# Optimization experiments

Hardware: AMD Instinct MI355X
Metric: run time of the kernel (lower is better)

The kernel has to match this reference:

```python
import jax, jax.numpy as jnp
import numpy as np

N_NODES = 50000
N_EDGES = 800000
D_IN = 512
D_OUT = 256


def setup_inputs() -> dict:
    key = jax.random.key(0)
    k1, k2, k3 = jax.random.split(key, 3)
    x = jax.random.normal(k1, (N_NODES, D_IN), dtype=jnp.float32)
    edge_index = jax.random.randint(k2, (2, N_EDGES), 0, N_NODES, dtype=jnp.int64)
    # Glorot-style init for the GCN weight, zero bias (PyG defaults)
    W = jax.random.normal(k3, (D_IN, D_OUT), dtype=jnp.float32) * (1.0 / np.sqrt(D_IN))
    b = jnp.zeros((D_OUT,), dtype=jnp.float32)
    return {"x": x, "edge_index": edge_index, "W": W, "b": b}


def reference(x, edge_index, W, b):
    N = x.shape[0]
    # 1) dense linear transform (the compute-heavy GEMM)
    xw = x @ W  # [N, d_out]

    # 2) add self-loops (PyG GCNConv default)
    loop = jnp.arange(N, dtype=edge_index.dtype)
    row = jnp.concatenate([edge_index[0], loop])  # sources
    col = jnp.concatenate([edge_index[1], loop])  # targets

    # 3) symmetric normalization deg^{-1/2} on targets (in-degree incl. self-loops)
    deg = jax.ops.segment_sum(jnp.ones_like(col, dtype=xw.dtype), col, num_segments=N)
    dinv = jnp.where(deg > 0, jax.lax.rsqrt(deg), 0.0)
    norm = dinv[row] * dinv[col]  # [E+N]

    # 4) gather source features, scale, scatter-add to targets
    msgs = xw[row] * norm[:, None]  # [E+N, d_out]
    agg = jax.ops.segment_sum(msgs, col, num_segments=N)  # [N, d_out]

    # 5) bias + ReLU (dropout is identity in eval mode)
    return jax.nn.relu(agg + b)
```

## Files before the change

kernel.cpp:

```cpp
#include <hip/hip_runtime.h>
#include <hip/hip_bf16.h>

#define N_NODES 50000
#define N_EDGES 800000
#define D_IN    512
#define D_OUT   256
#define NBLK_SCAN ((N_NODES + 1023) / 1024)
#define GEMM_NWG (((N_NODES + 127) / 128) * 2)
#define GEMM_Q   (GEMM_NWG / 8)
#define GEMM_R   (GEMM_NWG % 8)
#define GATH_CHUNKS ((N_NODES + 63) / 64)

typedef short s8v  __attribute__((ext_vector_type(8)));
typedef float f32x4 __attribute__((ext_vector_type(4)));

__device__ __forceinline__ unsigned short bf16b(float f) {
    __hip_bfloat16 h = __float2bfloat16(f);
    return *reinterpret_cast<unsigned short*>(&h);
}
__device__ __forceinline__ float bflo(unsigned u) { return __uint_as_float(u << 16); }
__device__ __forceinline__ float bfhi(unsigned u) { return __uint_as_float(u & 0xffff0000u); }

#define GLD16(gp, lp)                                                           \
    __builtin_amdgcn_global_load_lds(                                           \
        (const __attribute__((address_space(1))) unsigned int*)(const void*)(gp),\
        (__attribute__((address_space(3))) unsigned int*)(void*)(lp), 16, 0, 0)

__device__ __forceinline__ int wave_incl_scan(int v, int lane) {
    #pragma unroll
    for (int d = 1; d < 64; d <<= 1) {
        int u = __shfl_up(v, d, 64);
        if (lane >= d) v += u;
    }
    return v;
}

__global__ void k_wt(const float* __restrict__ W, unsigned short* __restrict__ Wt,
                     int* __restrict__ cnt4) {
    int k = blockIdx.x;
    int n = threadIdx.x;
    Wt[(size_t)n * D_IN + k] = bf16b(W[(size_t)k * D_OUT + n]);
    int t = (blockIdx.x * 256 + threadIdx.x) * 2;
    if (t < 4 * N_NODES) {
        cnt4[t] = 0;
        if (t + 1 < 4 * N_NODES) cnt4[t + 1] = 0;
    }
}


__global__ void k_count(const int* __restrict__ col, int* __restrict__ cnt4) {
    int i = (blockIdx.x * 256 + threadIdx.x) * 2;
    if (i < N_EDGES) {
        int2 c = *(const int2*)&col[i];
        atomicAdd(&cnt4[(i & 3) * N_NODES + c.x], 1);
        atomicAdd(&cnt4[((i + 1) & 3) * N_NODES + c.y], 1);
    }
}

__launch_bounds__(256)
__global__ void k_scan1(const int* __restrict__ cnt4, int* __restrict__ bsum) {
    const int t = threadIdx.x, b = blockIdx.x;
    const int idx = b * 1024 + t * 4;
    int s = 0;
    if (idx < N_NODES) {
        #pragma unroll
        for (int q = 0; q < 4; ++q) {
            int4 v = *(const int4*)&cnt4[q * N_NODES + idx];
            s += (v.x + v.y) + (v.z + v.w);
        }
    }
    #pragma unroll
    for (int d = 1; d < 64; d <<= 1) s += __shfl_xor(s, d, 64);
    __shared__ int ws[4];
    if ((t & 63) == 0) ws[t >> 6] = s;
    __syncthreads();
    if (t == 0) bsum[b] = ws[0] + ws[1] + ws[2] + ws[3];
}

__launch_bounds__(256)
__global__ void k_scan3(const int* __restrict__ cnt4, const int* __restrict__ bsum,
                        int* __restrict__ row_ptr, float* __restrict__ dinv,
                        int* __restrict__ cursor4) {
    const int t = threadIdx.x, b = blockIdx.x;
    const int lane = t & 63, wv = t >> 6;
    const int idx = b * 1024 + t * 4;
    int4 vq[4];
    int4 tot = make_int4(0, 0, 0, 0);
    if (idx < N_NODES) {
        #pragma unroll
        for (int q = 0; q < 4; ++q) {
            vq[q] = *(const int4*)&cnt4[q * N_NODES + idx];
            tot.x += vq[q].x; tot.y += vq[q].y;
            tot.z += vq[q].z; tot.w += vq[q].w;
        }
    } else {
        #pragma unroll
        for (int q = 0; q < 4; ++q) vq[q] = make_int4(0, 0, 0, 0);
    }
    int s = (tot.x + tot.y) + (tot.z + tot.w);
    int isc = wave_incl_scan(s, lane);
    __shared__ int wsum[4];
    __shared__ int s_boff;
    if (lane == 63) wsum[wv] = isc;
    if (t < 64) {
        int u = (t < b) ? bsum[t] : 0;
        #pragma unroll
        for (int d = 1; d < 64; d <<= 1) u += __shfl_xor(u, d, 64);
        if (t == 0) s_boff = u;
    }
    __syncthreads();
    int off = s_boff;
    #pragma unroll
    for (int i = 0; i < 4; ++i)
        if (i < wv) off += wsum[i];
    int p0 = off + isc - s;
    int p1 = p0 + tot.x;
    int p2 = p1 + tot.y;
    int p3 = p2 + tot.z;
    if (idx < N_NODES) {
        row_ptr[idx + 0] = p0; dinv[idx + 0] = rsqrtf(1.f + (float)tot.x);
        row_ptr[idx + 1] = p1; dinv[idx + 1] = rsqrtf(1.f + (float)tot.y);
        row_ptr[idx + 2] = p2; dinv[idx + 2] = rsqrtf(1.f + (float)tot.z);
        row_ptr[idx + 3] = p3; dinv[idx + 3] = rsqrtf(1.f + (float)tot.w);
        int4 run = make_int4(p0, p1, p2, p3);
        #pragma unroll
        for (int q = 0; q < 4; ++q) {
            *(int4*)&cursor4[q * N_NODES + idx] = run;
            run.x += vq[q].x; run.y += vq[q].y;
            run.z += vq[q].z; run.w += vq[q].w;
        }
    }
    if (b == 0 && t == 0) row_ptr[N_NODES] = N_EDGES;
}

__global__ void k_fill(const int* __restrict__ row, const int* __restrict__ col,
                       int* __restrict__ cursor4, int* __restrict__ csr_src) {
    int i = (blockIdx.x * 256 + threadIdx.x) * 2;
    if (i < N_EDGES) {
        int2 c = *(const int2*)&col[i];
        int2 r = *(const int2*)&row[i];
        int p0 = atomicAdd(&cursor4[(i & 3) * N_NODES + c.x], 1);
        csr_src[p0] = r.x;
        int p1 = atomicAdd(&cursor4[((i + 1) & 3) * N_NODES + c.y], 1);
        csr_src[p1] = r.y;
    }
}

__launch_bounds__(256)
__global__ void k_gemm(const float* __restrict__ A,
                       const unsigned short* __restrict__ Wt,
                       const float* __restrict__ dinv,
                       unsigned short* __restrict__ yb)
{
    __shared__ __align__(16) float          As[128 * 64];
    __shared__ __align__(16) unsigned short Bs[128 * 64];

    int orig = blockIdx.x;
    int xcd = orig % 8, pos = orig / 8;
    int wg = (xcd < GEMM_R) ? xcd * (GEMM_Q + 1) + pos
                            : GEMM_R * (GEMM_Q + 1) + (xcd - GEMM_R) * GEMM_Q + pos;
    const int nt = wg & 1;
    const int mt = wg >> 1;
    const int m0 = mt * 128;
    const int n0 = nt * 128;

    const int t  = threadIdx.x;
    const int w  = t >> 6;
    const int l  = t & 63;
    const int wm = (w >> 1) * 64;
    const int wn = (w & 1) * 64;
    const int lr = l & 15;
    const int lk = l >> 4;

    size_t aoff[8];
    #pragma unroll
    for (int i = 0; i < 8; ++i) {
        int row = m0 + w * 32 + i * 4 + (l >> 4);
        if (row >= N_NODES) row = 0;
        int sslot = (l & 15) ^ (row & 7);
        aoff[i] = (size_t)row * D_IN + sslot * 4;
    }
    const int srow = l >> 3;
    const int srcj = (l & 7) ^ srow;
    size_t boff[4];
    #pragma unroll
    for (int i = 0; i < 4; ++i) {
        int g = w * 4 + i;
        int bn = n0 + g * 8 + srow;
        boff[i] = (size_t)bn * D_IN + srcj * 8;
    }

    f32x4 acc[4][4] = {};

    for (int kk = 0; kk < D_IN; kk += 64) {
        #pragma unroll
        for (int i = 0; i < 8; ++i)
            GLD16(&A[aoff[i] + kk], (char*)As + (w * 32 + i * 4) * 256);
        #pragma unroll
        for (int i = 0; i < 4; ++i)
            GLD16(&Wt[boff[i] + kk], (char*)Bs + (w * 4 + i) * 1024);
        __syncthreads();

        #pragma unroll
        for (int ks = 0; ks < 2; ++ks) {
            s8v af[4], bfr[4];
            #pragma unroll
            for (int f = 0; f < 4; ++f) {
                int row = wm + f * 16 + lr;
                int a   = (ks * 4 + lk) * 2;
                int s0  = a ^ (lr & 7);
                int s1  = (a + 1) ^ (lr & 7);
                const char* pr = (const char*)As + row * 256;
                float4 x0 = *(const float4*)(pr + s0 * 16);
                float4 x1 = *(const float4*)(pr + s1 * 16);
                union { s8v v; unsigned short h[8]; } u;
                u.h[0] = bf16b(x0.x); u.h[1] = bf16b(x0.y);
                u.h[2] = bf16b(x0.z); u.h[3] = bf16b(x0.w);
                u.h[4] = bf16b(x1.x); u.h[5] = bf16b(x1.y);
                u.h[6] = bf16b(x1.z); u.h[7] = bf16b(x1.w);
                af[f] = u.v;
            }
            const int kb = (ks * 64 + lk * 16) ^ ((lr & 7) << 4);
            #pragma unroll
            for (int f = 0; f < 4; ++f)
                bfr[f] = *(const s8v*)((const char*)Bs + ((wn + f * 16 + lr) * 128 + kb));
            #pragma unroll
            for (int fm = 0; fm < 4; ++fm)
                #pragma unroll
                for (int fn = 0; fn < 4; ++fn)
                    acc[fm][fn] = __builtin_amdgcn_mfma_f32_16x16x32_bf16(
                        af[fm], bfr[fn], acc[fm][fn], 0, 0, 0);
        }
        __syncthreads();
    }

    #pragma unroll
    for (int fm = 0; fm < 4; ++fm) {
        #pragma unroll
        for (int j = 0; j < 4; ++j) {
            int row = m0 + wm + fm * 16 + lk * 4 + j;
            if (row < N_NODES) {
                float s = dinv[row];
                #pragma unroll
                for (int fn = 0; fn < 4; ++fn) {
                    int col = n0 + wn + fn * 16 + lr;
                    size_t off = (size_t)(col >> 5) * (N_NODES * 32)
                               + (size_t)row * 32 + (col & 31);
                    yb[off] = bf16b(acc[fm][fn][j] * s);
                }
            }
        }
    }
}

__device__ __forceinline__ void add8(float* acc, uint4 q) {
    unsigned x;
    x = q.x; acc[0] += bflo(x); acc[1] += bfhi(x);
    x = q.y; acc[2] += bflo(x); acc[3] += bfhi(x);
    x = q.z; acc[4] += bflo(x); acc[5] += bfhi(x);
    x = q.w; acc[6] += bflo(x); acc[7] += bfhi(x);
}

__launch_bounds__(256)
__global__ void k_gather(const int* __restrict__ row_ptr, const int* __restrict__ csr_src,
                         const unsigned short* __restrict__ yb,
                         const float* __restrict__ dinv,
                         const float* __restrict__ bias, float* __restrict__ out)
{
    const int s     = blockIdx.x & 7;
    const int chunk = blockIdx.x >> 3;
    const int g     = threadIdx.x >> 2;
    const int cs    = threadIdx.x & 3;
    const int c     = chunk * 64 + g;
    if (c >= N_NODES) return;

    const uint4* t4 = (const uint4*)(yb + (size_t)s * N_NODES * 32);

    float acc[8] = {0.f,0.f,0.f,0.f,0.f,0.f,0.f,0.f};

    const int e0 = row_ptr[c];
    const int e1 = row_ptr[c + 1];
    for (int i = e0; i < e1; i += 4) {
        int idx[4];
        #pragma unroll
        for (int j = 0; j < 4; ++j) {
            int p = i + j;
            idx[j] = csr_src[p < e1 ? p : e1 - 1];
        }
        uint4 v[4];
        #pragma unroll
        for (int j = 0; j < 4; ++j) v[j] = t4[(size_t)idx[j] * 4 + cs];
        #pragma unroll
        for (int j = 0; j < 4; ++j)
            if (i + j < e1) add8(acc, v[j]);
    }

    add8(acc, t4[(size_t)c * 4 + cs]);

    const float sc = dinv[c];
    const int colb = s * 32 + cs * 8;
    float4 b0 = *(const float4*)&bias[colb];
    float4 b1 = *(const float4*)&bias[colb + 4];
    float4 o0, o1;
    o0.x = fmaxf(fmaf(acc[0], sc, b0.x), 0.f);
    o0.y = fmaxf(fmaf(acc[1], sc, b0.y), 0.f);
    o0.z = fmaxf(fmaf(acc[2], sc, b0.z), 0.f);
    o0.w = fmaxf(fmaf(acc[3], sc, b0.w), 0.f);
    o1.x = fmaxf(fmaf(acc[4], sc, b1.x), 0.f);
    o1.y = fmaxf(fmaf(acc[5], sc, b1.y), 0.f);
    o1.z = fmaxf(fmaf(acc[6], sc, b1.z), 0.f);
    o1.w = fmaxf(fmaf(acc[7], sc, b1.w), 0.f);
    float* dst = &out[(size_t)c * D_OUT + colb];
    *(float4*)dst       = o0;
    *(float4*)(dst + 4) = o1;
}

extern "C" void kernel_launch(void* const* d_in, const int* in_sizes, int n_in,
                              void* d_out, int out_size, void* d_ws, size_t ws_size,
                              hipStream_t stream) {
    const float* x   = (const float*)d_in[0];
    const int*   ei  = (const int*)d_in[1];
    const float* W   = (const float*)d_in[2];
    const float* b   = (const float*)d_in[3];
    float*       out = (float*)d_out;

    const int* row = ei;
    const int* col = ei + N_EDGES;

    char* p = (char*)d_ws;
    unsigned short* yb = (unsigned short*)p;  p += (size_t)N_NODES * D_OUT * 2;
    unsigned short* Wt = (unsigned short*)p;  p += (size_t)D_OUT * D_IN * 2;
    int*   csr_src = (int*)p;                 p += (size_t)N_EDGES * 4;
    int*   cnt4    = (int*)p;                 p += (size_t)4 * N_NODES * 4;
    int*   row_ptr = (int*)p;                 p += (size_t)(N_NODES + 4) * 4;
    int*   cursor4 = (int*)p;                 p += (size_t)4 * N_NODES * 4;
    float* dinv    = (float*)p;               p += (size_t)N_NODES * 4;
    int*   bsum    = (int*)p;                 p += (size_t)NBLK_SCAN * 4;

    k_wt   <<<D_IN, D_OUT, 0, stream>>>(W, Wt, cnt4);
    k_count<<<(N_EDGES / 2 + 255) / 256, 256, 0, stream>>>(col, cnt4);
    k_scan1<<<NBLK_SCAN, 256, 0, stream>>>(cnt4, bsum);
    k_scan3<<<NBLK_SCAN, 256, 0, stream>>>(cnt4, bsum, row_ptr, dinv, cursor4);
    k_fill <<<(N_EDGES / 2 + 255) / 256, 256, 0, stream>>>(row, col, cursor4, csr_src);

    k_gemm<<<GEMM_NWG, 256, 0, stream>>>(x, Wt, dinv, yb);

    k_gather<<<GATH_CHUNKS * 8, 256, 0, stream>>>(row_ptr, csr_src, yb, dinv, b, out);
}
```

Before: 192.6 us.

## Assign one wavefront per destination node in gather with shuffle reduction

The gather kernel now maps a full 64-lane wavefront to each destination node and feature slice, with 16 edge slots of 4 lanes each, instead of 4 lanes per node. Each slot walks every 16th edge, with the next index prefetched one iteration ahead, and the partial sums are combined by xor shuffles. This is meant to expose more memory-level parallelism and spread the irregular degree load across lanes rather than serialising each node's edges. In exchange it launches 16x more threads, adds 32 shuffle adds per lane, and leaves most lanes idle on low-degree nodes. It also drops the bounds check and relies on N_NODES being divisible by 4.

```diff
diff --git a/kernel.cpp b/kernel.cpp
--- a/kernel.cpp
+++ b/kernel.cpp
@@ -9,7 +9,6 @@
 #define GEMM_NWG (((N_NODES + 127) / 128) * 2)
 #define GEMM_Q   (GEMM_NWG / 8)
 #define GEMM_R   (GEMM_NWG % 8)
-#define GATH_CHUNKS ((N_NODES + 63) / 64)
 
 typedef short s8v  __attribute__((ext_vector_type(8)));
 typedef float f32x4 __attribute__((ext_vector_type(4)));
@@ -267,52 +266,62 @@
                          const float* __restrict__ dinv,
                          const float* __restrict__ bias, float* __restrict__ out)
 {
-    const int s     = blockIdx.x & 7;
-    const int chunk = blockIdx.x >> 3;
-    const int g     = threadIdx.x >> 2;
-    const int cs    = threadIdx.x & 3;
-    const int c     = chunk * 64 + g;
-    if (c >= N_NODES) return;
+    const int s    = blockIdx.x & 7;
+    const int c    = (blockIdx.x >> 3) * 4 + (threadIdx.x >> 6);
+    const int l    = threadIdx.x & 63;
+    const int slot = l >> 2;
+    const int cs   = l & 3;
 
     const uint4* t4 = (const uint4*)(yb + (size_t)s * N_NODES * 32);
-
-    float acc[8] = {0.f,0.f,0.f,0.f,0.f,0.f,0.f,0.f};
 
     const int e0 = row_ptr[c];
     const int e1 = row_ptr[c + 1];
-    for (int i = e0; i < e1; i += 4) {
-        int idx[4];
-        #pragma unroll
-        for (int j = 0; j < 4; ++j) {
-            int p = i + j;
-            idx[j] = csr_src[p < e1 ? p : e1 - 1];
-        }
-        uint4 v[4];
-        #pragma unroll
-        for (int j = 0; j < 4; ++j) v[j] = t4[(size_t)idx[j] * 4 + cs];
-        #pragma unroll
-        for (int j = 0; j < 4; ++j)
-            if (i + j < e1) add8(acc, v[j]);
-    }
-
-    add8(acc, t4[(size_t)c * 4 + cs]);
-
-    const float sc = dinv[c];
-    const int colb = s * 32 + cs * 8;
-    float4 b0 = *(const float4*)&bias[colb];
-    float4 b1 = *(const float4*)&bias[colb + 4];
-    float4 o0, o1;
-    o0.x = fmaxf(fmaf(acc[0], sc, b0.x), 0.f);
-    o0.y = fmaxf(fmaf(acc[1], sc, b0.y), 0.f);
-    o0.z = fmaxf(fmaf(acc[2], sc, b0.z), 0.f);
-    o0.w = fmaxf(fmaf(acc[3], sc, b0.w), 0.f);
-    o1.x = fmaxf(fmaf(acc[4], sc, b1.x), 0.f);
-    o1.y = fmaxf(fmaf(acc[5], sc, b1.y), 0.f);
-    o1.z = fmaxf(fmaf(acc[6], sc, b1.z), 0.f);
-    o1.w = fmaxf(fmaf(acc[7], sc, b1.w), 0.f);
-    float* dst = &out[(size_t)c * D_OUT + colb];
-    *(float4*)dst       = o0;
-    *(float4*)(dst + 4) = o1;
+
+    uint4 sv = t4[(size_t)c * 4 + cs];
+
+    float acc[8] = {0.f,0.f,0.f,0.f,0.f,0.f,0.f,0.f};
+
+    int i = e0;
+    int idx = 0;
+    if (e1 > e0) {
+        int p = e0 + slot;
+        idx = csr_src[p < e1 ? p : e1 - 1];
+    }
+    while (i < e1) {
+        uint4 v = t4[(size_t)idx * 4 + cs];
+        int ni = i + 16;
+        int np = ni + slot;
+        int nidx = csr_src[np < e1 ? np : e1 - 1];
+        if (i + slot < e1) add8(acc, v);
+        i = ni;
+        idx = nidx;
+    }
+    if (slot == 0) add8(acc, sv);
+
+    #pragma unroll
+    for (int d = 4; d < 64; d <<= 1)
+        #pragma unroll
+        for (int u = 0; u < 8; ++u)
+            acc[u] += __shfl_xor(acc[u], d, 64);
+
+    if (slot == 0) {
+        const float sc = dinv[c];
+        const int colb = s * 32 + cs * 8;
+        float4 b0 = *(const float4*)&bias[colb];
+        float4 b1 = *(const float4*)&bias[colb + 4];
+        float4 o0, o1;
+        o0.x = fmaxf(fmaf(acc[0], sc, b0.x), 0.f);
+        o0.y = fmaxf(fmaf(acc[1], sc, b0.y), 0.f);
+        o0.z = fmaxf(fmaf(acc[2], sc, b0.z), 0.f);
+        o0.w = fmaxf(fmaf(acc[3], sc, b0.w), 0.f);
+        o1.x = fmaxf(fmaf(acc[4], sc, b1.x), 0.f);
+        o1.y = fmaxf(fmaf(acc[5], sc, b1.y), 0.f);
+        o1.z = fmaxf(fmaf(acc[6], sc, b1.z), 0.f);
+        o1.w = fmaxf(fmaf(acc[7], sc, b1.w), 0.f);
+        float* dst = &out[(size_t)c * D_OUT + colb];
+        *(float4*)dst       = o0;
+        *(float4*)(dst + 4) = o1;
+    }
 }
 
 extern "C" void kernel_launch(void* const* d_in, const int* in_sizes, int n_in,
@@ -345,5 +354,5 @@
 
     k_gemm<<<GEMM_NWG, 256, 0, stream>>>(x, Wt, dinv, yb);
 
-    k_gather<<<GATH_CHUNKS * 8, 256, 0, stream>>>(row_ptr, csr_src, yb, dinv, b, out);
-}
+    k_gather<<<(N_NODES / 4) * 8, 256, 0, stream>>>(row_ptr, csr_src, yb, dinv, b, out);
+}
```

Measured after the change: 267.9 us. 39.1% more time.

## Double-buffer GEMM K-tiles with async LDS loads and vmcnt waits

Applied to the files above, without the earlier changes.

Restructures the GEMM main loop from single-buffered 64-wide K tiles to double-buffered 32-wide K tiles. The next tile's global-to-LDS loads are issued while the current one is computed, and partial vmcnt waits with raw s_barrier replace full __syncthreads. The intent is to hide global load latency behind the MFMA work. In exchange it has twice as many barriers per K, new swizzle patterns, and relies on the hand-counted vmcnt being correct.

```diff
diff --git a/kernel.cpp b/kernel.cpp
--- a/kernel.cpp
+++ b/kernel.cpp
@@ -152,8 +152,8 @@
                        const float* __restrict__ dinv,
                        unsigned short* __restrict__ yb)
 {
-    __shared__ __align__(16) float          As[128 * 64];
-    __shared__ __align__(16) unsigned short Bs[128 * 64];
+    __shared__ __align__(16) float          As[2 * 128 * 32];
+    __shared__ __align__(16) unsigned short Bs[2 * 128 * 32];
 
     int orig = blockIdx.x;
     int xcd = orig % 8, pos = orig / 8;
@@ -172,67 +172,86 @@
     const int lr = l & 15;
     const int lk = l >> 4;
 
-    size_t aoff[8];
-    #pragma unroll
-    for (int i = 0; i < 8; ++i) {
-        int row = m0 + w * 32 + i * 4 + (l >> 4);
-        if (row >= N_NODES) row = 0;
-        int sslot = (l & 15) ^ (row & 7);
-        aoff[i] = (size_t)row * D_IN + sslot * 4;
-    }
-    const int srow = l >> 3;
-    const int srcj = (l & 7) ^ srow;
-    size_t boff[4];
+    size_t aoff[4];
     #pragma unroll
     for (int i = 0; i < 4; ++i) {
-        int g = w * 4 + i;
-        int bn = n0 + g * 8 + srow;
-        boff[i] = (size_t)bn * D_IN + srcj * 8;
+        int r = m0 + w * 32 + i * 8 + (l >> 3);
+        if (r >= N_NODES) r = 0;
+        aoff[i] = (size_t)r * D_IN + ((l & 7) ^ (l >> 3)) * 4;
+    }
+    size_t boff[2];
+    #pragma unroll
+    for (int i = 0; i < 2; ++i) {
+        int r = n0 + w * 32 + i * 16 + (l >> 2);
+        boff[i] = (size_t)r * D_IN + ((l & 3) ^ ((l >> 3) & 3)) * 8;
     }
 
     f32x4 acc[4][4] = {};
 
-    for (int kk = 0; kk < D_IN; kk += 64) {
-        #pragma unroll
-        for (int i = 0; i < 8; ++i)
-            GLD16(&A[aoff[i] + kk], (char*)As + (w * 32 + i * 4) * 256);
-        #pragma unroll
-        for (int i = 0; i < 4; ++i)
-            GLD16(&Wt[boff[i] + kk], (char*)Bs + (w * 4 + i) * 1024);
-        __syncthreads();
-
-        #pragma unroll
-        for (int ks = 0; ks < 2; ++ks) {
-            s8v af[4], bfr[4];
-            #pragma unroll
-            for (int f = 0; f < 4; ++f) {
-                int row = wm + f * 16 + lr;
-                int a   = (ks * 4 + lk) * 2;
-                int s0  = a ^ (lr & 7);
-                int s1  = (a + 1) ^ (lr & 7);
-                const char* pr = (const char*)As + row * 256;
-                float4 x0 = *(const float4*)(pr + s0 * 16);
-                float4 x1 = *(const float4*)(pr + s1 * 16);
-                union { s8v v; unsigned short h[8]; } u;
-                u.h[0] = bf16b(x0.x); u.h[1] = bf16b(x0.y);
-                u.h[2] = bf16b(x0.z); u.h[3] = bf16b(x0.w);
-                u.h[4] = bf16b(x1.x); u.h[5] = bf16b(x1.y);
-                u.h[6] = bf16b(x1.z); u.h[7] = bf16b(x1.w);
-                af[f] = u.v;
-            }
-            const int kb = (ks * 64 + lk * 16) ^ ((lr & 7) << 4);
-            #pragma unroll
-            for (int f = 0; f < 4; ++f)
-                bfr[f] = *(const s8v*)((const char*)Bs + ((wn + f * 16 + lr) * 128 + kb));
-            #pragma unroll
-            for (int fm = 0; fm < 4; ++fm)
-                #pragma unroll
-                for (int fn = 0; fn < 4; ++fn)
-                    acc[fm][fn] = __builtin_amdgcn_mfma_f32_16x16x32_bf16(
-                        af[fm], bfr[fn], acc[fm][fn], 0, 0, 0);
-        }
-        __syncthreads();
-    }
+    #define STAGE(buf, kk)                                                       \
+        do {                                                                     \
+            char* ab = (char*)As + (buf) * 16384 + w * 4096;                     \
+            char* bb = (char*)Bs + (buf) * 8192  + w * 2048;                     \
+            _Pragma("unroll")                                                    \
+            for (int i = 0; i < 4; ++i) GLD16(&A[aoff[i] + (kk)], ab + i * 1024);\
+            _Pragma("unroll")                                                    \
+            for (int i = 0; i < 2; ++i) GLD16(&Wt[boff[i] + (kk)], bb + i * 1024);\
+        } while (0)
+
+    #define COMPUTE(buf)                                                         \
+        do {                                                                     \
+            const char* abase = (const char*)As + (buf) * 16384;                 \
+            const char* bbase = (const char*)Bs + (buf) * 8192;                  \
+            s8v af[4], bfr[4];                                                   \
+            _Pragma("unroll")                                                    \
+            for (int f = 0; f < 4; ++f) {                                        \
+                int row = wm + f * 16 + lr;                   \
+                int s0  = (2 * lk) ^ (lr & 7);                                   \
+                const char* pr = abase + row * 128;                              \
+                float4 x0 = *(const float4*)(pr + s0 * 16);                      \
+                float4 x1 = *(const float4*)(pr + (s0 ^ 1) * 16);                \
+                union { s8v v; unsigned short h[8]; } u;                         \
+                u.h[0] = bf16b(x0.x); u.h[1] = bf16b(x0.y);                      \
+                u.h[2] = bf16b(x0.z); u.h[3] = bf16b(x0.w);                      \
+                u.h[4] = bf16b(x1.x); u.h[5] = bf16b(x1.y);                      \
+                u.h[6] = bf16b(x1.z); u.h[7] = bf16b(x1.w);                      \
+                af[f] = u.v;                                                     \
+            }                                                                    \
+            _Pragma("unroll")                                                    \
+            for (int f = 0; f < 4; ++f) {                                        \
+                int row = wn + f * 16 + lr;         \
+                int s   = lk ^ ((lr >> 1) & 3);                                  \
+                bfr[f] = *(const s8v*)(bbase + row * 64 + s * 16);               \
+            }                                                                    \
+            _Pragma("unroll")                                                    \
+            for (int fm = 0; fm < 4; ++fm)                                       \
+                _Pragma("unroll")                                                \
+                for (int fn = 0; fn < 4; ++fn)                                   \
+                    acc[fm][fn] = __builtin_amdgcn_mfma_f32_16x16x32_bf16(       \
+                        af[fm], bfr[fn], acc[fm][fn], 0, 0, 0);                  \
+        } while (0)
+
+    STAGE(0, 0);
+    STAGE(1, 32);
+    asm volatile("s_waitcnt vmcnt(6)" ::: "memory");
+    __builtin_amdgcn_s_barrier();
+
+    #pragma unroll 1
+    for (int tk = 0; tk < 14; ++tk) {
+        COMPUTE(tk & 1);
+        __builtin_amdgcn_s_barrier();
+        STAGE(tk & 1, (tk + 2) * 32);
+        asm volatile("s_waitcnt vmcnt(6)" ::: "memory");
+        __builtin_amdgcn_s_barrier();
+    }
+    COMPUTE(0);
+    __builtin_amdgcn_s_barrier();
+    asm volatile("s_waitcnt vmcnt(0)" ::: "memory");
+    __builtin_amdgcn_s_barrier();
+    COMPUTE(1);
+
+    #undef STAGE
+    #undef COMPUTE
 
     #pragma unroll
     for (int fm = 0; fm < 4; ++fm) {
```

Result: no change. 193.1 us (+0.3%).

## Fuse CSR fill into GEMM launch as interleaved blocks; unroll gather by 8

Applied to the files above, without the earlier changes.

Moves the edge-fill (atomic cursor scatter into csr_src) into the GEMM kernel. Every fourth block acts as a persistent grid-stride fill worker, so the fill runs concurrently with the GEMM blocks and one launch and its serial dependency disappear. The gather inner loop now processes 8 neighbors per iteration instead of 4, which puts more independent loads in flight. The cost is fill blocks competing with GEMM blocks for CU slots and memory bandwidth, plus higher register use in the gather loop.

```diff
diff --git a/kernel.cpp b/kernel.cpp
--- a/kernel.cpp
+++ b/kernel.cpp
@@ -9,6 +9,8 @@
 #define GEMM_NWG (((N_NODES + 127) / 128) * 2)
 #define GEMM_Q   (GEMM_NWG / 8)
 #define GEMM_R   (GEMM_NWG % 8)
+#define FILL_NB  260
+#define FUSE_NB  (GEMM_NWG + FILL_NB)
 #define GATH_CHUNKS ((N_NODES + 63) / 64)
 
 typedef short s8v  __attribute__((ext_vector_type(8)));
@@ -133,30 +135,37 @@
     if (b == 0 && t == 0) row_ptr[N_NODES] = N_EDGES;
 }
 
-__global__ void k_fill(const int* __restrict__ row, const int* __restrict__ col,
-                       int* __restrict__ cursor4, int* __restrict__ csr_src) {
-    int i = (blockIdx.x * 256 + threadIdx.x) * 2;
-    if (i < N_EDGES) {
-        int2 c = *(const int2*)&col[i];
-        int2 r = *(const int2*)&row[i];
-        int p0 = atomicAdd(&cursor4[(i & 3) * N_NODES + c.x], 1);
-        csr_src[p0] = r.x;
-        int p1 = atomicAdd(&cursor4[((i + 1) & 3) * N_NODES + c.y], 1);
-        csr_src[p1] = r.y;
-    }
-}
-
 __launch_bounds__(256)
 __global__ void k_gemm(const float* __restrict__ A,
                        const unsigned short* __restrict__ Wt,
                        const float* __restrict__ dinv,
-                       unsigned short* __restrict__ yb)
+                       unsigned short* __restrict__ yb,
+                       const int* __restrict__ row, const int* __restrict__ col,
+                       int* __restrict__ cursor4, int* __restrict__ csr_src)
 {
     __shared__ __align__(16) float          As[128 * 64];
     __shared__ __align__(16) unsigned short Bs[128 * 64];
 
-    int orig = blockIdx.x;
-    int xcd = orig % 8, pos = orig / 8;
+    const int bid = blockIdx.x;
+    const int t   = threadIdx.x;
+
+    if ((bid & 3) == 3) {
+        const int cid = bid >> 2;
+        const int stride = FILL_NB * 256 * 2;
+        for (int i = (cid * 256 + t) * 2; i < N_EDGES; i += stride) {
+            int2 c = *(const int2*)&col[i];
+            int2 r = *(const int2*)&row[i];
+            int p0 = atomicAdd(&cursor4[(i & 3) * N_NODES + c.x], 1);
+            csr_src[p0] = r.x;
+            int p1 = atomicAdd(&cursor4[((i + 1) & 3) * N_NODES + c.y], 1);
+            csr_src[p1] = r.y;
+        }
+        return;
+    }
+
+    const int gid = bid - (bid >> 2);
+
+    int xcd = gid % 8, pos = gid / 8;
     int wg = (xcd < GEMM_R) ? xcd * (GEMM_Q + 1) + pos
                             : GEMM_R * (GEMM_Q + 1) + (xcd - GEMM_R) * GEMM_Q + pos;
     const int nt = wg & 1;
@@ -164,7 +173,6 @@
     const int m0 = mt * 128;
     const int n0 = nt * 128;
 
-    const int t  = threadIdx.x;
     const int w  = t >> 6;
     const int l  = t & 63;
     const int wm = (w >> 1) * 64;
@@ -175,10 +183,10 @@
     size_t aoff[8];
     #pragma unroll
     for (int i = 0; i < 8; ++i) {
-        int row = m0 + w * 32 + i * 4 + (l >> 4);
-        if (row >= N_NODES) row = 0;
-        int sslot = (l & 15) ^ (row & 7);
-        aoff[i] = (size_t)row * D_IN + sslot * 4;
+        int rw = m0 + w * 32 + i * 4 + (l >> 4);
+        if (rw >= N_NODES) rw = 0;
+        int sslot = (l & 15) ^ (rw & 7);
+        aoff[i] = (size_t)rw * D_IN + sslot * 4;
     }
     const int srow = l >> 3;
     const int srcj = (l & 7) ^ srow;
@@ -206,11 +214,11 @@
             s8v af[4], bfr[4];
             #pragma unroll
             for (int f = 0; f < 4; ++f) {
-                int row = wm + f * 16 + lr;
-                int a   = (ks * 4 + lk) * 2;
-                int s0  = a ^ (lr & 7);
-                int s1  = (a + 1) ^ (lr & 7);
-                const char* pr = (const char*)As + row * 256;
+                int rw = wm + f * 16 + lr;
+                int a  = (ks * 4 + lk) * 2;
+                int s0 = a ^ (lr & 7);
+                int s1 = (a + 1) ^ (lr & 7);
+                const char* pr = (const char*)As + rw * 256;
                 float4 x0 = *(const float4*)(pr + s0 * 16);
                 float4 x1 = *(const float4*)(pr + s1 * 16);
                 union { s8v v; unsigned short h[8]; } u;
@@ -238,14 +246,14 @@
     for (int fm = 0; fm < 4; ++fm) {
         #pragma unroll
         for (int j = 0; j < 4; ++j) {
-            int row = m0 + wm + fm * 16 + lk * 4 + j;
-            if (row < N_NODES) {
-                float s = dinv[row];
+            int rw = m0 + wm + fm * 16 + lk * 4 + j;
+            if (rw < N_NODES) {
+                float s = dinv[rw];
                 #pragma unroll
                 for (int fn = 0; fn < 4; ++fn) {
-                    int col = n0 + wn + fn * 16 + lr;
-                    size_t off = (size_t)(col >> 5) * (N_NODES * 32)
-                               + (size_t)row * 32 + (col & 31);
+                    int cl = n0 + wn + fn * 16 + lr;
+                    size_t off = (size_t)(cl >> 5) * (N_NODES * 32)
+                               + (size_t)rw * 32 + (cl & 31);
                     yb[off] = bf16b(acc[fm][fn][j] * s);
                 }
             }
@@ -280,18 +288,18 @@
 
     const int e0 = row_ptr[c];
     const int e1 = row_ptr[c + 1];
-    for (int i = e0; i < e1; i += 4) {
-        int idx[4];
-        #pragma unroll
-        for (int j = 0; j < 4; ++j) {
+    for (int i = e0; i < e1; i += 8) {
+        int idx[8];
+        #pragma unroll
+        for (int j = 0; j < 8; ++j) {
             int p = i + j;
             idx[j] = csr_src[p < e1 ? p : e1 - 1];
         }
-        uint4 v[4];
-        #pragma unroll
-        for (int j = 0; j < 4; ++j) v[j] = t4[(size_t)idx[j] * 4 + cs];
-        #pragma unroll
-        for (int j = 0; j < 4; ++j)
+        uint4 v[8];
+        #pragma unroll
+        for (int j = 0; j < 8; ++j) v[j] = t4[(size_t)idx[j] * 4 + cs];
+        #pragma unroll
+        for (int j = 0; j < 8; ++j)
             if (i + j < e1) add8(acc, v[j]);
     }
 
@@ -341,9 +349,8 @@
     k_count<<<(N_EDGES / 2 + 255) / 256, 256, 0, stream>>>(col, cnt4);
     k_scan1<<<NBLK_SCAN, 256, 0, stream>>>(cnt4, bsum);
     k_scan3<<<NBLK_SCAN, 256, 0, stream>>>(cnt4, bsum, row_ptr, dinv, cursor4);
-    k_fill <<<(N_EDGES / 2 + 255) / 256, 256, 0, stream>>>(row, col, cursor4, csr_src);
-
-    k_gemm<<<GEMM_NWG, 256, 0, stream>>>(x, Wt, dinv, yb);
+
+    k_gemm<<<FUSE_NB, 256, 0, stream>>>(x, Wt, dinv, yb, row, col, cursor4, csr_src);
 
     k_gather<<<GATH_CHUNKS * 8, 256, 0, stream>>>(row_ptr, csr_src, yb, dinv, b, out);
 }
```

Result: faster. 187.7 us (-2.5%).
